# Kernel tuning notes

Hardware: AMD Instinct MI355X
Metric: run time of the kernel (lower is better)

The kernel has to match this reference:

```python
import jax, jax.numpy as jnp
import numpy as np

B = 262144  # batch size
# fast-weight slice boundaries: 3*10=30, 10*10=100, 10*1=10 -> total 140
S1, S2, S3 = 30, 130, 140


def setup_inputs() -> dict:
    key = jax.random.key(0)
    k1, k2, k3, k4, k5 = jax.random.split(key, 5)
    return {
        "x": jax.random.normal(k1, (B, 1, 3), dtype=jnp.float32),
        "update": jax.random.normal(k2, (B, 140, 1), dtype=jnp.float32),
        "W1": jax.random.normal(k3, (3, 10), dtype=jnp.float32),
        "W2": jax.random.normal(k4, (10, 10), dtype=jnp.float32),
        "W3": jax.random.normal(k5, (10, 1), dtype=jnp.float32),
    }


def _squash(W, u):
    # weight.weight = sigmoid(10 * (W + u - 0.5))
    return jax.nn.sigmoid(10.0 * (W + u - 0.5))


def reference(x, update, W1, W2, W3):
    xs = x[:, 0, :]          # [B, 3]
    us = update[:, :, 0]     # [B, 140]

    def step(carry, inp):
        w1, w2, w3 = carry
        xi, ui = inp  # xi: [3], ui: [140]
        w1 = _squash(w1, ui[:S1].reshape(3, 10))
        w2 = _squash(w2, ui[S1:S2].reshape(10, 10))
        w3 = _squash(w3, ui[S2:S3].reshape(10, 1))
        h = jnp.tanh(xi @ w1)   # [10]
        h = jnp.tanh(h @ w2)    # [10]
        y = h @ w3              # [1]
        return (w1, w2, w3), y

    _, preds = jax.lax.scan(step, (W1, W2, W3), (xs, us))
    return preds  # [B, 1]
```

## Files before the change

### kernel.cpp

```cpp
#include <hip/hip_runtime.h>
#include <hip/hip_fp16.h>

typedef _Float16 h2 __attribute__((ext_vector_type(2)));
typedef float f2 __attribute__((ext_vector_type(2)));

#define NCH   1024
#define CL    256
#define HALO  32
#define SPB   8
#define NB    ((HALO + CL) / SPB)
#define BH    (HALO / SPB)
#define DEPTH 6
#define UBUF_DW (SPB * 140)
#define TROW  141
#define NROWS 16

#if __has_builtin(__builtin_amdgcn_exp2f)
#define EXP2F __builtin_amdgcn_exp2f
#else
#define EXP2F exp2f
#endif
#if __has_builtin(__builtin_amdgcn_rcpf)
#define RCPF __builtin_amdgcn_rcpf
#else
#define RCPF(x) (1.0f / (x))
#endif

#define A_K   (-14.4269504088896341f)
#define UPC_K (7.21347520444481704f)
#define K2_K  (2.8853900817779268f)

__device__ __forceinline__ h2 pkrtz(float a, float b) {
    return __builtin_bit_cast(h2, __builtin_amdgcn_cvt_pkrtz(a, b));
}
__device__ __forceinline__ float sigstep(float w, float up) {
    return RCPF(1.0f + EXP2F(__builtin_fmaf(A_K, w, up)));
}
__device__ __forceinline__ float fold(float u) {
    return __builtin_fmaf(A_K, u, UPC_K);
}
__device__ __forceinline__ uint32_t pk16(float a, float b) {
    return __builtin_bit_cast(uint32_t, pkrtz(a, b));
}
__device__ __forceinline__ h2 ldw(uint32_t v) {
    return __builtin_bit_cast(h2, v);
}
__device__ __forceinline__ h2 tanh2(h2 a) {
    float z0 = (float)a[0], z1 = (float)a[1];
    float t0 = 1.0f - 2.0f * RCPF(1.0f + EXP2F(K2_K * z0));
    float t1 = 1.0f - 2.0f * RCPF(1.0f + EXP2F(K2_K * z1));
    return pkrtz(t0, t1);
}

__device__ __forceinline__ void gload_lds16(const float* g, float* l) {
    __builtin_amdgcn_global_load_lds(
        (__attribute__((address_space(1))) void*)(void*)g,
        (__attribute__((address_space(3))) void*)(void*)l, 16, 0, 0);
}
__device__ __forceinline__ void gload_lds4(const float* g, float* l) {
    __builtin_amdgcn_global_load_lds(
        (__attribute__((address_space(1))) void*)(void*)g,
        (__attribute__((address_space(3))) void*)(void*)l, 4, 0, 0);
}

#define STR2(x) #x
#define WAITVMn(N) asm volatile("s_waitcnt vmcnt(" STR2(N) ")" ::: "memory")
#define WAITLGKM   asm volatile("s_waitcnt lgkmcnt(0)" ::: "memory")

__global__ void __launch_bounds__(64)
fastnet_kernel(const float* __restrict__ x, const float* __restrict__ u,
               const float* __restrict__ W1, const float* __restrict__ W2,
               const float* __restrict__ W3, float* __restrict__ out) {
    __shared__ __align__(16) float    ubuf_s[DEPTH * UBUF_DW];
    __shared__ __align__(16) uint32_t traj[NROWS * TROW];
    __shared__ __align__(16) float    xbuf_s[3 * 96];

    const int  lane  = threadIdx.x;
    const int  ch    = blockIdx.x;
    const long cbase = (long)ch * CL;
    const float* su  = u + (cbase - (long)HALO) * 140;
    float* ubuf0 = ubuf_s;
    float* xbuf0 = xbuf_s;

    float wa, wb, wc;
    if (ch == 0) {
        wa = (lane < 30) ? W1[lane] : (lane < 130 ? W2[lane - 30] : W3[lane - 130]);
        wb = W2[lane + 34];
        int kc = lane + 128;
        wc = (lane < 12) ? ((kc < 130) ? W2[kc - 30] : W3[kc - 130]) : 0.5f;
    } else {
        wa = wb = wc = 0.5f;
    }

#define STAGE(B_) do {                                                          \
        const float* s_ = su + (long)(B_) * UBUF_DW;                            \
        float* d_ = ubuf0 + ((B_) % DEPTH) * UBUF_DW;                           \
        _Pragma("unroll")                                                       \
        for (int i_ = 0; i_ < 4; i_++)                                          \
            gload_lds16(s_ + i_ * 256 + lane * 4, d_ + i_ * 256);               \
        gload_lds4(s_ + 1024 + lane, d_ + 1024);                                \
        if (lane < 32) gload_lds4(s_ + 1088 + lane, d_ + 1088);                 \
        if ((B_) >= BH && (((B_) - BH) & 3) == 0) {                             \
            int r_ = ((B_) - BH) >> 2;                                          \
            if (lane < 24)                                                      \
                gload_lds16(x + (cbase + r_ * 32) * 3 + lane * 4,               \
                            xbuf0 + (r_ % 3) * 96 + lane * 4);                  \
        }                                                                       \
    } while (0)

#define ITER(B_, NW_, POS_, TRAJ_, PB_, STG_) do {                              \
        WAITVMn(NW_);                                                           \
        const float* ub_ = ubuf0 + ((B_) % DEPTH) * UBUF_DW;                    \
        float uu0[SPB], uu1[SPB], uu2[SPB];                                     \
        _Pragma("unroll")                                                       \
        for (int t = 0; t < SPB; t++) {                                         \
            uu0[t] = ub_[t * 140 + lane];                                       \
            uu1[t] = ub_[t * 140 + 64 + lane];                                  \
            uu2[t] = ub_[t * 140 + 128 + (lane < 12 ? lane : 11)];              \
        }                                                                       \
        WAITLGKM;                         \
        if (STG_) STAGE((B_) + DEPTH);                                          \
        _Pragma("unroll")                                                       \
        for (int t = 0; t < SPB; t += 2) {                                      \
            wa = sigstep(wa, fold(uu0[t]));                                     \
            wb = sigstep(wb, fold(uu1[t]));                                     \
            wc = sigstep(wc, fold(uu2[t]));                                     \
            float wa0 = wa, wb0 = wb, wc0 = wc;                                 \
            wa = sigstep(wa, fold(uu0[t + 1]));                                 \
            wb = sigstep(wb, fold(uu1[t + 1]));                                 \
            wc = sigstep(wc, fold(uu2[t + 1]));                                 \
            if (TRAJ_) {                                                        \
                uint32_t* tw = &traj[((POS_) * 4 + (t >> 1)) * TROW + lane];    \
                tw[0]  = pk16(wa0, wa);                                         \
                tw[64] = pk16(wb0, wb);                                         \
                if (lane < 12) tw[128] = pk16(wc0, wc);                         \
            }                                                                   \
        }                                                                       \
        if (PB_ && lane < NROWS) {                                              \
            int r_ = ((B_) - (BH + 3)) >> 2;                                    \
            const float* xb_ = xbuf0 + (r_ % 3) * 96 + 6 * lane;                \
            f2 v0 = *(const f2*)(xb_);                                          \
            f2 v1 = *(const f2*)(xb_ + 2);                                      \
            f2 v2 = *(const f2*)(xb_ + 4);                                      \
            h2 xq0 = pkrtz(v0[0], v1[1]);                                       \
            h2 xq1 = pkrtz(v0[1], v2[0]);                                       \
            h2 xq2 = pkrtz(v1[0], v2[1]);                                       \
            const uint32_t* tr_ = &traj[lane * TROW];                           \
            h2 h1[10];                                                          \
            _Pragma("unroll")                                                   \
            for (int cc = 0; cc < 10; cc++) {                                   \
                h2 acc = ldw(tr_[cc]) * xq0;                                    \
                acc += ldw(tr_[10 + cc]) * xq1;                                 \
                acc += ldw(tr_[20 + cc]) * xq2;                                 \
                h1[cc] = tanh2(acc);                                            \
            }                                                                   \
            h2 hh[10];                                                          \
            _Pragma("unroll")                                                   \
            for (int cc = 0; cc < 10; cc++) {                                   \
                h2 acc = h1[0] * ldw(tr_[30 + cc]);                             \
                _Pragma("unroll")                                               \
                for (int r2 = 1; r2 < 10; r2++)                                 \
                    acc += h1[r2] * ldw(tr_[30 + r2 * 10 + cc]);                \
                hh[cc] = tanh2(acc);                                            \
            }                                                                   \
            h2 ya = hh[0] * ldw(tr_[130]);                                      \
            _Pragma("unroll")                                                   \
            for (int r2 = 1; r2 < 10; r2++) ya += hh[r2] * ldw(tr_[130 + r2]);  \
            long g0_ = cbase + r_ * 32 + 2 * lane;                              \
            f2 o_; o_[0] = (float)ya[0]; o_[1] = (float)ya[1];                  \
            *reinterpret_cast<f2*>(out + g0_) = o_;                             \
        }                                                                       \
    } while (0)

    const int b0 = (ch == 0) ? BH : 0;
    for (int i = 0; i < DEPTH; i++) STAGE(b0 + i);

    if (ch != 0) {
        ITER(0, 31, 0, 0, 0, 1);
        ITER(1, 31, 1, 0, 0, 1);
        ITER(2, 31, 2, 0, 0, 1);
        ITER(3, 32, 3, 0, 0, 1);
    }

    for (int rb = BH; rb <= 24; rb += 4) {
        ITER(rb + 0, 31, 0, 1, 0, 1);
        ITER(rb + 1, 31, 1, 1, 0, 1);
        ITER(rb + 2, 31, 2, 1, 0, 1);
        ITER(rb + 3, 32, 3, 1, 1, 1);
    }

    ITER(28, 31, 0, 1, 0, 1);
    ITER(29, 31, 1, 1, 0, 1);
    ITER(30, 31, 2, 1, 0, 0);
    ITER(31, 25, 3, 1, 1, 0);
    ITER(32, 18, 0, 1, 0, 0);
    ITER(33, 12, 1, 1, 0, 0);
    ITER(34,  6, 2, 1, 0, 0);
    ITER(35,  0, 3, 1, 1, 0);

#undef STAGE
#undef ITER
}

extern "C" void kernel_launch(void* const* d_in, const int* in_sizes, int n_in,
                              void* d_out, int out_size, void* d_ws, size_t ws_size,
                              hipStream_t stream) {
    const float* x  = (const float*)d_in[0];
    const float* u  = (const float*)d_in[1];
    const float* W1 = (const float*)d_in[2];
    const float* W2 = (const float*)d_in[3];
    const float* W3 = (const float*)d_in[4];
    float* out = (float*)d_out;

    hipLaunchKernelGGL(fastnet_kernel, dim3(NCH), dim3(64), 0, stream,
                       x, u, W1, W2, W3, out);
}
```

Before: 45.04 us.

## Replace LDS-staged pipeline with register triple-buffered loads and smaller chunks

Halves the chunk length to 128 and doubles the number of chunks (2048 blocks), which doubles the relative halo recompute but raises parallelism. The global_load_lds ring buffer in shared memory is replaced by direct global-to-register loads, triple-buffered across three register sets two blocks ahead, with vmcnt waits. x is also loaded straight into registers, and outputs are emitted every two blocks for 16 rows using 8 lanes. This removes the LDS staging and its lgkm waits at the cost of more registers and more redundant halo work.

```diff
diff --git a/kernel.cpp b/kernel.cpp
--- a/kernel.cpp
+++ b/kernel.cpp
@@ -4,16 +4,13 @@
 typedef _Float16 h2 __attribute__((ext_vector_type(2)));
 typedef float f2 __attribute__((ext_vector_type(2)));
 
-#define NCH   1024
-#define CL    256
+#define NCH   2048
+#define CL    128
 #define HALO  32
 #define SPB   8
-#define NB    ((HALO + CL) / SPB)
-#define BH    (HALO / SPB)
-#define DEPTH 6
-#define UBUF_DW (SPB * 140)
+#define NB    20
+#define BH    4
 #define TROW  141
-#define NROWS 16
 
 #if __has_builtin(__builtin_amdgcn_exp2f)
 #define EXP2F __builtin_amdgcn_exp2f
@@ -52,35 +49,20 @@
     return pkrtz(t0, t1);
 }
 
-__device__ __forceinline__ void gload_lds16(const float* g, float* l) {
-    __builtin_amdgcn_global_load_lds(
-        (__attribute__((address_space(1))) void*)(void*)g,
-        (__attribute__((address_space(3))) void*)(void*)l, 16, 0, 0);
-}
-__device__ __forceinline__ void gload_lds4(const float* g, float* l) {
-    __builtin_amdgcn_global_load_lds(
-        (__attribute__((address_space(1))) void*)(void*)g,
-        (__attribute__((address_space(3))) void*)(void*)l, 4, 0, 0);
-}
-
 #define STR2(x) #x
 #define WAITVMn(N) asm volatile("s_waitcnt vmcnt(" STR2(N) ")" ::: "memory")
-#define WAITLGKM   asm volatile("s_waitcnt lgkmcnt(0)" ::: "memory")
 
 __global__ void __launch_bounds__(64)
 fastnet_kernel(const float* __restrict__ x, const float* __restrict__ u,
                const float* __restrict__ W1, const float* __restrict__ W2,
                const float* __restrict__ W3, float* __restrict__ out) {
-    __shared__ __align__(16) float    ubuf_s[DEPTH * UBUF_DW];
-    __shared__ __align__(16) uint32_t traj[NROWS * TROW];
-    __shared__ __align__(16) float    xbuf_s[3 * 96];
+    __shared__ uint32_t traj[8 * TROW];
 
     const int  lane  = threadIdx.x;
     const int  ch    = blockIdx.x;
     const long cbase = (long)ch * CL;
     const float* su  = u + (cbase - (long)HALO) * 140;
-    float* ubuf0 = ubuf_s;
-    float* xbuf0 = xbuf_s;
+    const int  cl    = (lane < 12) ? lane : 11;
 
     float wa, wb, wc;
     if (ch == 0) {
@@ -92,59 +74,54 @@
         wa = wb = wc = 0.5f;
     }
 
-#define STAGE(B_) do {                                                          \
-        const float* s_ = su + (long)(B_) * UBUF_DW;                            \
-        float* d_ = ubuf0 + ((B_) % DEPTH) * UBUF_DW;                           \
-        _Pragma("unroll")                                                       \
-        for (int i_ = 0; i_ < 4; i_++)                                          \
-            gload_lds16(s_ + i_ * 256 + lane * 4, d_ + i_ * 256);               \
-        gload_lds4(s_ + 1024 + lane, d_ + 1024);                                \
-        if (lane < 32) gload_lds4(s_ + 1088 + lane, d_ + 1088);                 \
-        if ((B_) >= BH && (((B_) - BH) & 3) == 0) {                             \
-            int r_ = ((B_) - BH) >> 2;                                          \
-            if (lane < 24)                                                      \
-                gload_lds16(x + (cbase + r_ * 32) * 3 + lane * 4,               \
-                            xbuf0 + (r_ % 3) * 96 + lane * 4);                  \
-        }                                                                       \
-    } while (0)
-
-#define ITER(B_, NW_, POS_, TRAJ_, PB_, STG_) do {                              \
-        WAITVMn(NW_);                                                           \
-        const float* ub_ = ubuf0 + ((B_) % DEPTH) * UBUF_DW;                    \
-        float uu0[SPB], uu1[SPB], uu2[SPB];                                     \
+    float aU0[SPB], aU1[SPB], aU2[SPB];
+    float bU0[SPB], bU1[SPB], bU2[SPB];
+    float cU0[SPB], cU1[SPB], cU2[SPB];
+    f2 xE[3], xO[3];
+
+#define ISSUE_L(B_, U0, U1, U2) do {                                            \
+        const float* p_ = su + (long)(B_) * (SPB * 140);                        \
         _Pragma("unroll")                                                       \
         for (int t = 0; t < SPB; t++) {                                         \
-            uu0[t] = ub_[t * 140 + lane];                                       \
-            uu1[t] = ub_[t * 140 + 64 + lane];                                  \
-            uu2[t] = ub_[t * 140 + 128 + (lane < 12 ? lane : 11)];              \
-        }                                                                       \
-        WAITLGKM;                         \
-        if (STG_) STAGE((B_) + DEPTH);                                          \
+            U0[t] = p_[t * 140 + lane];                                         \
+            U1[t] = p_[t * 140 + 64 + lane];                                    \
+            U2[t] = p_[t * 140 + 128 + cl];                                     \
+        }                                                                       \
+    } while (0)
+
+#define ISSUE_X(R_, XS_) do {                                                   \
+        if (lane < 8) {                                                         \
+            const float* xp_ = x + (cbase + (long)(R_) * 16 + 2 * lane) * 3;    \
+            XS_[0] = *(const f2*)(xp_);                                         \
+            XS_[1] = *(const f2*)(xp_ + 2);                                     \
+            XS_[2] = *(const f2*)(xp_ + 4);                                     \
+        }                                                                       \
+    } while (0)
+
+#define BLK(B_, N_, UC0, UC1, UC2, UL0, UL1, UL2, XR_, XSI_, PBR_, XSC_, TRAJ_) do { \
+        if ((XR_) >= 0) ISSUE_X(XR_, XSI_);                                     \
+        if ((B_) + 2 < NB) ISSUE_L((B_) + 2, UL0, UL1, UL2);                    \
+        WAITVMn(N_);                                                            \
         _Pragma("unroll")                                                       \
         for (int t = 0; t < SPB; t += 2) {                                      \
-            wa = sigstep(wa, fold(uu0[t]));                                     \
-            wb = sigstep(wb, fold(uu1[t]));                                     \
-            wc = sigstep(wc, fold(uu2[t]));                                     \
+            wa = sigstep(wa, fold(UC0[t]));                                     \
+            wb = sigstep(wb, fold(UC1[t]));                                     \
+            wc = sigstep(wc, fold(UC2[t]));                                     \
             float wa0 = wa, wb0 = wb, wc0 = wc;                                 \
-            wa = sigstep(wa, fold(uu0[t + 1]));                                 \
-            wb = sigstep(wb, fold(uu1[t + 1]));                                 \
-            wc = sigstep(wc, fold(uu2[t + 1]));                                 \
+            wa = sigstep(wa, fold(UC0[t + 1]));                                 \
+            wb = sigstep(wb, fold(UC1[t + 1]));                                 \
+            wc = sigstep(wc, fold(UC2[t + 1]));                                 \
             if (TRAJ_) {                                                        \
-                uint32_t* tw = &traj[((POS_) * 4 + (t >> 1)) * TROW + lane];    \
+                uint32_t* tw = &traj[((((B_) - BH) & 1) * 4 + (t >> 1)) * TROW + lane]; \
                 tw[0]  = pk16(wa0, wa);                                         \
                 tw[64] = pk16(wb0, wb);                                         \
                 if (lane < 12) tw[128] = pk16(wc0, wc);                         \
             }                                                                   \
         }                                                                       \
-        if (PB_ && lane < NROWS) {                                              \
-            int r_ = ((B_) - (BH + 3)) >> 2;                                    \
-            const float* xb_ = xbuf0 + (r_ % 3) * 96 + 6 * lane;                \
-            f2 v0 = *(const f2*)(xb_);                                          \
-            f2 v1 = *(const f2*)(xb_ + 2);                                      \
-            f2 v2 = *(const f2*)(xb_ + 4);                                      \
-            h2 xq0 = pkrtz(v0[0], v1[1]);                                       \
-            h2 xq1 = pkrtz(v0[1], v2[0]);                                       \
-            h2 xq2 = pkrtz(v1[0], v2[1]);                                       \
+        if ((PBR_) >= 0 && lane < 8) {                                          \
+            h2 xq0 = pkrtz(XSC_[0][0], XSC_[1][1]);                             \
+            h2 xq1 = pkrtz(XSC_[0][1], XSC_[2][0]);                             \
+            h2 xq2 = pkrtz(XSC_[1][0], XSC_[2][1]);                             \
             const uint32_t* tr_ = &traj[lane * TROW];                           \
             h2 h1[10];                                                          \
             _Pragma("unroll")                                                   \
@@ -166,40 +143,48 @@
             h2 ya = hh[0] * ldw(tr_[130]);                                      \
             _Pragma("unroll")                                                   \
             for (int r2 = 1; r2 < 10; r2++) ya += hh[r2] * ldw(tr_[130 + r2]);  \
-            long g0_ = cbase + r_ * 32 + 2 * lane;                              \
+            long g0_ = cbase + (long)(PBR_) * 16 + 2 * lane;                    \
             f2 o_; o_[0] = (float)ya[0]; o_[1] = (float)ya[1];                  \
             *reinterpret_cast<f2*>(out + g0_) = o_;                             \
         }                                                                       \
     } while (0)
 
-    const int b0 = (ch == 0) ? BH : 0;
-    for (int i = 0; i < DEPTH; i++) STAGE(b0 + i);
-
     if (ch != 0) {
-        ITER(0, 31, 0, 0, 0, 1);
-        ITER(1, 31, 1, 0, 0, 1);
-        ITER(2, 31, 2, 0, 0, 1);
-        ITER(3, 32, 3, 0, 0, 1);
+        ISSUE_L(0, aU0, aU1, aU2);
+        ISSUE_L(1, bU0, bU1, bU2);
+    } else {
+        ISSUE_X(0, xE);
+        ISSUE_L(4, bU0, bU1, bU2);
+        ISSUE_L(5, cU0, cU1, cU2);
     }
 
-    for (int rb = BH; rb <= 24; rb += 4) {
-        ITER(rb + 0, 31, 0, 1, 0, 1);
-        ITER(rb + 1, 31, 1, 1, 0, 1);
-        ITER(rb + 2, 31, 2, 1, 0, 1);
-        ITER(rb + 3, 32, 3, 1, 1, 1);
+    if (ch != 0) {
+        BLK(0, 48, aU0,aU1,aU2, cU0,cU1,cU2, -1, xE, -1, xE, 0);
+        BLK(1, 48, bU0,bU1,bU2, aU0,aU1,aU2, -1, xE, -1, xE, 0);
+        BLK(2, 48, cU0,cU1,cU2, bU0,bU1,bU2, -1, xE, -1, xE, 0);
+        BLK(3, 51, aU0,aU1,aU2, cU0,cU1,cU2,  0, xE, -1, xE, 0);
     }
 
-    ITER(28, 31, 0, 1, 0, 1);
-    ITER(29, 31, 1, 1, 0, 1);
-    ITER(30, 31, 2, 1, 0, 0);
-    ITER(31, 25, 3, 1, 1, 0);
-    ITER(32, 18, 0, 1, 0, 0);
-    ITER(33, 12, 1, 1, 0, 0);
-    ITER(34,  6, 2, 1, 0, 0);
-    ITER(35,  0, 3, 1, 1, 0);
-
-#undef STAGE
-#undef ITER
+    BLK( 4, 48, bU0,bU1,bU2, aU0,aU1,aU2, -1, xE, -1, xE, 1);
+    BLK( 5, 51, cU0,cU1,cU2, bU0,bU1,bU2,  1, xO,  0, xE, 1);
+    BLK( 6, 51, aU0,aU1,aU2, cU0,cU1,cU2, -1, xE, -1, xE, 1);
+    BLK( 7, 51, bU0,bU1,bU2, aU0,aU1,aU2,  2, xE,  1, xO, 1);
+    BLK( 8, 51, cU0,cU1,cU2, bU0,bU1,bU2, -1, xE, -1, xE, 1);
+    BLK( 9, 51, aU0,aU1,aU2, cU0,cU1,cU2,  3, xO,  2, xE, 1);
+    BLK(10, 51, bU0,bU1,bU2, aU0,aU1,aU2, -1, xE, -1, xE, 1);
+    BLK(11, 51, cU0,cU1,cU2, bU0,bU1,bU2,  4, xE,  3, xO, 1);
+    BLK(12, 51, aU0,aU1,aU2, cU0,cU1,cU2, -1, xE, -1, xE, 1);
+    BLK(13, 51, bU0,bU1,bU2, aU0,aU1,aU2,  5, xO,  4, xE, 1);
+    BLK(14, 51, cU0,cU1,cU2, bU0,bU1,bU2, -1, xE, -1, xE, 1);
+    BLK(15, 51, aU0,aU1,aU2, cU0,cU1,cU2,  6, xE,  5, xO, 1);
+    BLK(16, 51, bU0,bU1,bU2, aU0,aU1,aU2, -1, xE, -1, xE, 1);
+    BLK(17, 51, cU0,cU1,cU2, bU0,bU1,bU2,  7, xO,  6, xE, 1);
+    BLK(18, 27, aU0,aU1,aU2, cU0,cU1,cU2, -1, xE, -1, xE, 1);
+    BLK(19,  0, bU0,bU1,bU2, aU0,aU1,aU2, -1, xE,  7, xO, 1);
+
+#undef ISSUE_L
+#undef ISSUE_X
+#undef BLK
 }
 
 extern "C" void kernel_launch(void* const* d_in, const int* in_sizes, int n_in,
```

Result: slower. 46.21 us (+2.6%).
